# Kernel optimization log

Measured on AMD Instinct MI355X. Metric: run time of the kernel, lower is better.

Reference implementation:

```python
import jax, jax.numpy as jnp
import numpy as np
import math

EPS = 1e-5
GROUPS = 8


def setup_inputs() -> dict:
    key = jax.random.key(0)
    ks = jax.random.split(key, 4)
    b, c, h, w = 4, 256, 64, 64
    x = jax.random.normal(ks[0], (b, c, h, w), dtype=jnp.float32)
    norm_w = jnp.ones((c,), dtype=jnp.float32)
    norm_b = jnp.zeros((c,), dtype=jnp.float32)
    qkv_w = jax.random.normal(ks[1], (3 * c, c), dtype=jnp.float32) * (1.0 / math.sqrt(c))
    qkv_b = jnp.zeros((3 * c,), dtype=jnp.float32)
    proj_w = jax.random.normal(ks[2], (c, c), dtype=jnp.float32) * (1.0 / math.sqrt(c))
    proj_b = jnp.zeros((c,), dtype=jnp.float32)
    return {"x": x, "norm_w": norm_w, "norm_b": norm_b, "qkv_w": qkv_w,
            "qkv_b": qkv_b, "proj_w": proj_w, "proj_b": proj_b}


def group_norm(x, weight, bias):
    b, c, h, w = x.shape
    xg = x.reshape(b, GROUPS, c // GROUPS, h, w)
    mean = xg.mean(axis=(2, 3, 4), keepdims=True)
    var = xg.var(axis=(2, 3, 4), keepdims=True)
    xg = (xg - mean) * jax.lax.rsqrt(var + EPS)
    xn = xg.reshape(b, c, h, w)
    return xn * weight[None, :, None, None] + bias[None, :, None, None]


def reference(x, norm_w, norm_b, qkv_w, qkv_b, proj_w, proj_b):
    b, c, h, w = x.shape
    n = h * w
    xn = group_norm(x, norm_w, norm_b)
    # 1x1 conv == per-pixel linear: tokens [b, n, c]
    tokens = xn.reshape(b, c, n).transpose(0, 2, 1)
    qkv = jnp.einsum('bnc,oc->bno', tokens, qkv_w) + qkv_b  # [b, n, 3c]
    q, k, v = jnp.split(qkv, 3, axis=-1)
    scale = 1.0 / math.sqrt(c)
    attn = jnp.einsum('bqc,bkc->bqk', q, k) * scale  # [b, n, n]
    attn = jax.nn.softmax(attn, axis=-1)
    out = jnp.einsum('bqk,bkc->bqc', attn, v)  # [b, n, c]
    out = jnp.einsum('bnc,oc->bno', out, proj_w) + proj_b
    out = out.transpose(0, 2, 1).reshape(b, c, h, w)
    return x + out
```

## Files before the change

### kernel.cpp

```cpp
#include <hip/hip_runtime.h>
#include <math.h>

typedef unsigned short u16;
typedef __bf16 bf16x8 __attribute__((ext_vector_type(8)));
typedef u16    u16x8  __attribute__((ext_vector_type(8)));
typedef float  f32x4  __attribute__((ext_vector_type(4)));
typedef float  f32x16 __attribute__((ext_vector_type(16)));

__device__ __forceinline__ float b2f(u16 u) {
    union { unsigned u; float f; } x; x.u = ((unsigned)u) << 16; return x.f;
}
__device__ __forceinline__ u16 f2b(float f) {
    union { float f; unsigned u; } x; x.f = f;
    unsigned r = x.u + 0x7FFFu + ((x.u >> 16) & 1u);
    return (u16)(r >> 16);
}
__device__ __forceinline__ f32x4 mfma16(bf16x8 a, bf16x8 b, f32x4 c) {
    return __builtin_amdgcn_mfma_f32_16x16x32_bf16(a, b, c, 0, 0, 0);
}
__device__ __forceinline__ f32x16 mfma32(bf16x8 a, bf16x8 b, f32x16 c) {
    return __builtin_amdgcn_mfma_f32_32x32x16_bf16(a, b, c, 0, 0, 0);
}
__device__ __forceinline__ void dma16(const void* g, void* l) {
    __builtin_amdgcn_global_load_lds((const __attribute__((address_space(1))) void*)g,
                                     (__attribute__((address_space(3))) void*)l, 16, 0, 0);
}
__device__ __forceinline__ int dtype_vote(const unsigned* w) {
    unsigned v = w[threadIdx.x & 63];
    unsigned e = ((v & 0xFFFFu) >> 7) & 0xFFu;
    unsigned long long m = __ballot(e >= 0x60u && e <= 0x8Fu);
    return (__popcll(m) >= 32) ? 0 : 1;
}

#define QSCALE 0.09016844f

__global__ __launch_bounds__(256) void k_cvtx(const void* __restrict__ src, u16* __restrict__ dst,
                                              int* __restrict__ flag, float2* __restrict__ part) {
    const int f = dtype_vote((const unsigned*)src);
    if (blockIdx.x == 0 && threadIdx.x == 0) *flag = f;
    const int i = (blockIdx.x * 256 + threadIdx.x) * 4;
    u16 o[4];
    if (f) {
        float4 v = *(const float4*)((const float*)src + i);
        o[0] = f2b(v.x); o[1] = f2b(v.y); o[2] = f2b(v.z); o[3] = f2b(v.w);
    } else {
        uint2 v = *(const uint2*)((const u16*)src + i);
        o[0] = (u16)(v.x & 0xFFFF); o[1] = (u16)(v.x >> 16);
        o[2] = (u16)(v.y & 0xFFFF); o[3] = (u16)(v.y >> 16);
    }
    unsigned lo = (unsigned)o[0] | ((unsigned)o[1] << 16);
    unsigned hi = (unsigned)o[2] | ((unsigned)o[3] << 16);
    *(uint2*)(dst + i) = make_uint2(lo, hi);
    float s = 0.f, ss = 0.f;
#pragma unroll
    for (int e = 0; e < 4; e++) { float x = b2f(o[e]); s += x; ss += x * x; }
#pragma unroll
    for (int d = 1; d < 64; d <<= 1) { s += __shfl_xor(s, d, 64); ss += __shfl_xor(ss, d, 64); }
    __shared__ float rs[4], rss[4];
    const int wv = threadIdx.x >> 6;
    if ((threadIdx.x & 63) == 0) { rs[wv] = s; rss[wv] = ss; }
    __syncthreads();
    if (threadIdx.x == 0)
        part[blockIdx.x] = make_float2(rs[0] + rs[1] + rs[2] + rs[3],
                                       rss[0] + rss[1] + rss[2] + rss[3]);
}

__global__ __launch_bounds__(64) void k_statsf(const float2* __restrict__ part, float* __restrict__ stats) {
    const int g = blockIdx.x, lane = threadIdx.x;
    float2 a = part[g * 128 + lane], b = part[g * 128 + 64 + lane];
    float s = a.x + b.x, ss = a.y + b.y;
#pragma unroll
    for (int d = 1; d < 64; d <<= 1) { s += __shfl_xor(s, d, 64); ss += __shfl_xor(ss, d, 64); }
    if (lane == 0) {
        float mean = s * (1.f / 131072.f);
        float var = fmaxf(ss * (1.f / 131072.f) - mean * mean, 0.f);
        stats[g] = mean;
        stats[32 + g] = rsqrtf(var + 1e-5f);
    }
}

__global__ __launch_bounds__(256) void k_cvtp(const void* s0, const void* s1, const void* s2,
                                              const void* s3, const void* s4, const void* s5,
                                              u16* d0, u16* d1, u16* d2, u16* d3, u16* d4, u16* d5) {
    const int f = dtype_vote((const unsigned*)s2);
    const int i = blockIdx.x * 256 + threadIdx.x;
    const void* s; u16* d; int j;
    if      (i < 256)    { s = s0; d = d0; j = i; }
    else if (i < 512)    { s = s1; d = d1; j = i - 256; }
    else if (i < 197120) { s = s2; d = d2; j = i - 512; }
    else if (i < 197888) { s = s3; d = d3; j = i - 197120; }
    else if (i < 263424) { s = s4; d = d4; j = i - 197888; }
    else if (i < 263680) { s = s5; d = d5; j = i - 263424; }
    else return;
    if (f) d[j] = f2b(((const float*)s)[j]);
    else   d[j] = ((const u16*)s)[j];
}

__global__ __launch_bounds__(256) void k_tok(const u16* __restrict__ x, const u16* __restrict__ nw,
                                             const u16* __restrict__ nb, const float* __restrict__ stats,
                                             u16* __restrict__ tok) {
    const int b = blockIdx.z, c0 = blockIdx.y * 64, p0 = blockIdx.x * 64;
    __shared__ u16 t[64][72];
    const int cl = threadIdx.x >> 2, seg = threadIdx.x & 3;
    const int c = c0 + cl;
    const int g = c >> 5;
    const float mean = stats[b * 8 + g], rstd = stats[32 + b * 8 + g];
    const float scale = b2f(nw[c]) * rstd;
    const float shift = b2f(nb[c]) - mean * scale;
    const u16* xp = x + ((size_t)(b * 256 + c)) * 4096 + p0 + seg * 16;
#pragma unroll
    for (int h = 0; h < 2; h++) {
        bf16x8 v = *(const bf16x8*)(xp + h * 8);
#pragma unroll
        for (int j = 0; j < 8; j++)
            t[seg * 16 + h * 8 + j][cl] = f2b((float)v[j] * scale + shift);
    }
    __syncthreads();
    u16x8 o0, o1;
#pragma unroll
    for (int j = 0; j < 8; j++) { o0[j] = t[cl][seg * 16 + j]; o1[j] = t[cl][seg * 16 + 8 + j]; }
    u16* op = tok + ((size_t)(b * 4096 + p0 + cl)) * 256 + c0 + seg * 16;
    *(u16x8*)op = o0;
    *((u16x8*)op + 1) = o1;
}

__global__ __launch_bounds__(256) void k_qkv(const u16* __restrict__ A, const u16* __restrict__ W,
                                             const u16* __restrict__ bias,
                                             u16* __restrict__ Qo, u16* __restrict__ Ko, u16* __restrict__ Vt) {
    const int m0 = blockIdx.x * 128, n0 = blockIdx.y * 128;
    const int cls = blockIdx.y >> 1, sub = (blockIdx.y & 1) * 128;
    const int b = m0 >> 12, p0 = m0 & 4095;
    const int tid = threadIdx.x, w = tid >> 6, lane = tid & 63, l15 = lane & 15, l4 = lane >> 4;
    const int wm = w >> 1, wn = w & 1;
    __shared__ __attribute__((aligned(16))) char QL[32768];
    u16* At = (u16*)QL;
    u16* Bt = (u16*)(QL + 16384);
    u16* E  = (u16*)QL;
    f32x4 acc[4][4];
    const f32x4 z = {0.f, 0.f, 0.f, 0.f};
#pragma unroll
    for (int i = 0; i < 4; i++)
#pragma unroll
        for (int j = 0; j < 4; j++) acc[i][j] = z;

    for (int kt = 0; kt < 4; kt++) {
        const int k0 = kt * 64;
#pragma unroll
        for (int i = 0; i < 4; i++) {
            int v = tid + i * 256;
            int row = v >> 3, c8 = v & 7;
            int swz = (c8 ^ (row & 7)) << 3;
            *(u16x8*)(&At[row * 64 + swz]) = *(const u16x8*)(A + (size_t)(m0 + row) * 256 + k0 + c8 * 8);
            *(u16x8*)(&Bt[row * 64 + swz]) = *(const u16x8*)(W + (size_t)(n0 + row) * 256 + k0 + c8 * 8);
        }
        __syncthreads();
#pragma unroll
        for (int ks = 0; ks < 2; ks++) {
            const int sc = ((ks * 4 + l4) ^ (l15 & 7)) << 3;
            bf16x8 af[4], bfr[4];
#pragma unroll
            for (int i = 0; i < 4; i++) {
                af[i]  = *(const bf16x8*)(&At[(wm * 64 + i * 16 + l15) * 64 + sc]);
                bfr[i] = *(const bf16x8*)(&Bt[(wn * 64 + i * 16 + l15) * 64 + sc]);
            }
#pragma unroll
            for (int i = 0; i < 4; i++)
#pragma unroll
                for (int j = 0; j < 4; j++) acc[i][j] = mfma16(af[i], bfr[j], acc[i][j]);
        }
        __syncthreads();
    }

    const float sf = (cls == 0) ? QSCALE : 1.f;
#pragma unroll
    for (int j = 0; j < 4; j++) {
        const int nl = wn * 64 + j * 16 + l15;
        const float bia = b2f(bias[n0 + nl]);
#pragma unroll
        for (int i = 0; i < 4; i++) {
#pragma unroll
            for (int r = 0; r < 4; r++) {
                const int ml = wm * 64 + i * 16 + l4 * 4 + r;
                const u16 val = f2b((acc[i][j][r] + bia) * sf);
                if (cls < 2) {
                    E[ml * 128 + (((nl >> 3) ^ (ml & 7)) << 3) + (nl & 7)] = val;
                } else {
                    int ps = ml ^ ((((ml >> 2) ^ (ml >> 3)) & 1) * 12);
                    E[nl * 128 + (((ps >> 3) ^ (nl & 7)) << 3) + (ps & 7)] = val;
                }
            }
        }
    }
    __syncthreads();
    const int row = tid >> 1, half = tid & 1;
    if (cls < 2) {
        u16* dst = (cls == 0 ? Qo : Ko) + (size_t)(m0 + row) * 256 + sub;
#pragma unroll
        for (int k = 0; k < 8; k++) {
            const int chunk = half * 8 + k;
            u16x8 v = *(const u16x8*)(&E[row * 128 + ((chunk ^ (row & 7)) << 3)]);
            *(u16x8*)(dst + chunk * 8) = v;
        }
    } else {
        u16* dst = Vt + (size_t)(b * 256 + sub + row) * 4096 + p0;
#pragma unroll
        for (int k = 0; k < 8; k++) {
            const int chunk = half * 8 + k;
            u16x8 v = *(const u16x8*)(&E[row * 128 + ((chunk ^ (row & 7)) << 3)]);
            *(u16x8*)(dst + chunk * 8) = v;
        }
    }
}

__global__ __launch_bounds__(256, 2) void k_attn(const u16* __restrict__ Q, const u16* __restrict__ K,
                                                 const u16* __restrict__ Vt,
                                                 u16* __restrict__ Up, float* __restrict__ ml) {
    const int qt = blockIdx.x, b = blockIdx.y, sp = blockIdx.z;
    const int tid = threadIdx.x, w = tid >> 6, lane = tid & 63;
    const int l31 = lane & 31, h = lane >> 5;
    const int qcol = qt * 128 + w * 32 + l31;

    __shared__ __attribute__((aligned(16))) char LB[65536];
    u16* KT = (u16*)LB;
    u16* VT = (u16*)(LB + 16384);

    bf16x8 aq[16];
    {
        const u16* qp = Q + ((size_t)(b * 4096 + qcol)) * 256 + h * 8;
#pragma unroll
        for (int kb = 0; kb < 16; kb++) aq[kb] = *(const bf16x8*)(qp + kb * 16);
    }
    f32x16 acc[8];
#pragma unroll
    for (int ct = 0; ct < 8; ct++)
#pragma unroll
        for (int r = 0; r < 16; r++) acc[ct][r] = 0.f;
    float m_i = -3e38f, l_i = 0.f;

    const u16* Kg0 = K + (size_t)(b * 4096 + sp * 1024) * 256;
    const u16* Vg0 = Vt + (size_t)b * 256 * 4096 + sp * 1024;
    const int wb = (tid & 192) * 8;

    for (int kt = 0; kt < 32; kt++) {
        {
            const u16* Kg = Kg0 + (size_t)kt * 32 * 256;
#pragma unroll
            for (int i = 0; i < 4; i++) {
                int q = i * 256 + tid;
                int row = q >> 5, c = q & 31;
                dma16(Kg + row * 256 + ((c ^ row) << 3), &KT[i * 2048 + wb]);
            }
            const u16* Vg = Vg0 + kt * 32;
#pragma unroll
            for (int i = 0; i < 4; i++) {
                int q = i * 256 + tid;
                int row = q >> 2, c = q & 3;
                dma16(Vg + (size_t)row * 4096 + ((c ^ ((row >> 3) & 3)) << 3), &VT[i * 2048 + wb]);
            }
        }
        __syncthreads();

        f32x16 st;
#pragma unroll
        for (int r = 0; r < 16; r++) st[r] = 0.f;
#pragma unroll
        for (int kb = 0; kb < 16; kb++) {
            bf16x8 bk = *(const bf16x8*)(&KT[l31 * 256 + (((kb * 2 + h) ^ l31) << 3)]);
            st = mfma32(bk, aq[kb], st);
        }

        float mx = st[0];
#pragma unroll
        for (int r = 1; r < 16; r++) mx = fmaxf(mx, st[r]);
        mx = fmaxf(mx, __shfl_xor(mx, 32, 64));
        if (__any(mx > m_i + 4.f)) {
            const float m_new = fmaxf(m_i, mx);
            const float al = __builtin_amdgcn_exp2f(m_i - m_new);
#pragma unroll
            for (int ct = 0; ct < 8; ct++)
#pragma unroll
                for (int r = 0; r < 16; r++) acc[ct][r] *= al;
            l_i *= al;
            m_i = m_new;
        }
        float sum = 0.f;
#pragma unroll
        for (int r = 0; r < 16; r++) {
            st[r] = __builtin_amdgcn_exp2f(st[r] - m_i);
            sum += st[r];
        }
        sum += __shfl_xor(sum, 32, 64);
        l_i += sum;

        union { u16x8 u; bf16x8 bv; } p0, p1;
#pragma unroll
        for (int e = 0; e < 8; e++) { p0.u[e] = f2b(st[e]); p1.u[e] = f2b(st[8 + e]); }

#pragma unroll
        for (int ct = 0; ct < 8; ct++) {
            bf16x8 av0 = *(const bf16x8*)(&VT[(ct * 32 + l31) * 32 + ((h ^ (l31 >> 3)) << 3)]);
            acc[ct] = mfma32(av0, p0.bv, acc[ct]);
            bf16x8 av1 = *(const bf16x8*)(&VT[(ct * 32 + l31) * 32 + (((2 + h) ^ (l31 >> 3)) << 3)]);
            acc[ct] = mfma32(av1, p1.bv, acc[ct]);
        }
        __syncthreads();
    }

    if (h == 0)
        ((float2*)ml)[(size_t)(sp * 4 + b) * 4096 + qcol] = make_float2(m_i, l_i);
    u16* Ot = (u16*)(LB + w * 16384);
#pragma unroll
    for (int ct = 0; ct < 8; ct++) {
#pragma unroll
        for (int r = 0; r < 16; r++) {
            const int c = ct * 32 + (r & 3) + 8 * (r >> 2) + 4 * h;
            Ot[l31 * 256 + (((c >> 3) ^ l31) << 3) + (c & 7)] = f2b(acc[ct][r]);
        }
    }
    u16* up = Up + ((size_t)(sp * 4 + b) * 4096 + qt * 128 + w * 32) * 256;
#pragma unroll
    for (int v = 0; v < 16; v++) {
        int idx = v * 64 + lane;
        int qrow = idx >> 5, c8 = idx & 31;
        u16x8 d = *(const u16x8*)(&Ot[qrow * 256 + ((c8 ^ qrow) << 3)]);
        *(u16x8*)(up + (size_t)qrow * 256 + c8 * 8) = d;
    }
}

__global__ __launch_bounds__(256) void k_proj(const u16* __restrict__ Up, const float* __restrict__ ml,
                                              const u16* __restrict__ W, const u16* __restrict__ bias,
                                              const u16* __restrict__ x, void* __restrict__ out,
                                              const int* __restrict__ flag) {
    const int f32out = *flag;
    const int m0 = blockIdx.x * 64;
    const int b = m0 >> 12, q0 = m0 & 4095;
    const int tid = threadIdx.x, w = tid >> 6, lane = tid & 63, l15 = lane & 15, l4 = lane >> 4;
    const int wm = w >> 1, wn = w & 1;
    __shared__ __attribute__((aligned(16))) char PL[40960];
    u16* At = (u16*)PL;
    u16* Bt = (u16*)(PL + 8192);
    u16* Ot = (u16*)PL;
    __shared__ float4 W4s[64];

    if (tid < 64) {
        const int q = q0 + tid;
        float m_s[4], l_s[4];
#pragma unroll
        for (int s = 0; s < 4; s++) {
            float2 v = ((const float2*)ml)[(size_t)(s * 4 + b) * 4096 + q];
            m_s[s] = v.x; l_s[s] = v.y;
        }
        float M = fmaxf(fmaxf(m_s[0], m_s[1]), fmaxf(m_s[2], m_s[3]));
        float L = 0.f, e[4];
#pragma unroll
        for (int s = 0; s < 4; s++) { e[s] = __builtin_amdgcn_exp2f(m_s[s] - M); L += l_s[s] * e[s]; }
        float inv = 1.f / fmaxf(L, 1e-30f);
        W4s[tid] = make_float4(e[0] * inv, e[1] * inv, e[2] * inv, e[3] * inv);
    }
    __syncthreads();

    const int qa = tid >> 2, ca = (tid & 3) * 16;
    const float4 wq = W4s[qa];
    const float wsv[4] = {wq.x, wq.y, wq.z, wq.w};
    const u16* upb = Up + (size_t)(q0 + qa) * 256 + ca;

    f32x4 acc[2][8];
    const f32x4 z = {0.f, 0.f, 0.f, 0.f};
#pragma unroll
    for (int i = 0; i < 2; i++)
#pragma unroll
        for (int j = 0; j < 8; j++) acc[i][j] = z;

    for (int kt = 0; kt < 4; kt++) {
        const int k0 = kt * 64;
        {
            float vs[16];
#pragma unroll
            for (int e = 0; e < 16; e++) vs[e] = 0.f;
#pragma unroll
            for (int s = 0; s < 4; s++) {
                const u16* p = upb + ((size_t)(s * 4 + b) * 4096) * 256 + k0;
                u16x8 u0 = *(const u16x8*)p;
                u16x8 u1 = *(const u16x8*)(p + 8);
                const float ws = wsv[s];
#pragma unroll
                for (int e = 0; e < 8; e++) { vs[e] += b2f(u0[e]) * ws; vs[8 + e] += b2f(u1[e]) * ws; }
            }
            u16x8 o0, o1;
#pragma unroll
            for (int e = 0; e < 8; e++) { o0[e] = f2b(vs[e]); o1[e] = f2b(vs[8 + e]); }
            const int c8 = ca >> 3;
            *(u16x8*)(&At[qa * 64 + ((c8 ^ (qa & 7)) << 3)]) = o0;
            *(u16x8*)(&At[qa * 64 + (((c8 + 1) ^ (qa & 7)) << 3)]) = o1;
        }
#pragma unroll
        for (int i = 0; i < 8; i++) {
            int v = i * 256 + tid;
            int row = v >> 3, c8 = v & 7;
            *(u16x8*)(&Bt[row * 64 + ((c8 ^ (row & 7)) << 3)]) =
                *(const u16x8*)(W + (size_t)row * 256 + k0 + c8 * 8);
        }
        __syncthreads();
#pragma unroll
        for (int ks = 0; ks < 2; ks++) {
            const int sc = ((ks * 4 + l4) ^ (l15 & 7)) << 3;
            bf16x8 af[2], bfr[8];
#pragma unroll
            for (int i = 0; i < 2; i++)
                af[i] = *(const bf16x8*)(&At[(wm * 32 + i * 16 + l15) * 64 + sc]);
#pragma unroll
            for (int j = 0; j < 8; j++)
                bfr[j] = *(const bf16x8*)(&Bt[(wn * 128 + j * 16 + l15) * 64 + sc]);
#pragma unroll
            for (int i = 0; i < 2; i++)
#pragma unroll
                for (int j = 0; j < 8; j++) acc[i][j] = mfma16(af[i], bfr[j], acc[i][j]);
        }
        __syncthreads();
    }

#pragma unroll
    for (int j = 0; j < 8; j++) {
        const int n = wn * 128 + j * 16 + l15;
        const float bia = b2f(bias[n]);
#pragma unroll
        for (int i = 0; i < 2; i++) {
#pragma unroll
            for (int r = 0; r < 4; r++) {
                const int p = wm * 32 + i * 16 + l4 * 4 + r;
                Ot[n * 64 + ((((p >> 3) ^ (n & 7)) << 3)) + (p & 7)] = f2b(acc[i][j][r] + bia);
            }
        }
    }
    __syncthreads();
    const int ps = (tid & 7) * 8;
#pragma unroll
    for (int v = 0; v < 8; v++) {
        const int n = v * 32 + (tid >> 3);
        u16x8 d = *(const u16x8*)(&Ot[n * 64 + ((((ps >> 3) ^ (n & 7)) << 3))]);
        const size_t base = ((size_t)(b * 256 + n)) * 4096 + q0 + ps;
        u16x8 xv = *(const u16x8*)(x + base);
        if (f32out) {
            float4 o0, o1;
#pragma unroll
            for (int e = 0; e < 4; e++) o0[e] = b2f(d[e]) + b2f(xv[e]);
#pragma unroll
            for (int e = 0; e < 4; e++) o1[e] = b2f(d[4 + e]) + b2f(xv[4 + e]);
            *(float4*)((float*)out + base) = o0;
            *(float4*)((float*)out + base + 4) = o1;
        } else {
            u16x8 o;
#pragma unroll
            for (int e = 0; e < 8; e++) o[e] = f2b(b2f(d[e]) + b2f(xv[e]));
            *(u16x8*)((u16*)out + base) = o;
        }
    }
}

extern "C" void kernel_launch(void* const* d_in, const int* in_sizes, int n_in,
                              void* d_out, int out_size, void* d_ws, size_t ws_size,
                              hipStream_t stream) {
    char* ws = (char*)d_ws;
    float* stats = (float*)ws;
    int*   flag  = (int*)(ws + 2048);
    float2* part = (float2*)(ws + 4096);
    u16* xb  = (u16*)(ws + 65536);
    u16* nwb = xb + (size_t)4194304;
    u16* nbb = nwb + 256;
    u16* qbb = nbb + 256;
    u16* pbb = qbb + 768;
    u16* pad = pbb + 256;
    u16* qwb = pad + 256;
    u16* pwb = qwb + (size_t)196608;
    u16* tok = pwb + (size_t)65536;
    u16* Qb  = tok + (size_t)16384 * 256;
    u16* Kb  = Qb  + (size_t)16384 * 256;
    u16* Vb  = Kb  + (size_t)16384 * 256;
    u16* Upb = Vb  + (size_t)16384 * 256;
    float* mlb = (float*)(Upb + (size_t)16 * 4096 * 256);

    k_cvtx  <<<dim3(4096), dim3(256), 0, stream>>>(d_in[0], xb, flag, part);
    k_statsf<<<dim3(32), dim3(64), 0, stream>>>(part, stats);
    k_cvtp  <<<dim3(1030), dim3(256), 0, stream>>>(d_in[1], d_in[2], d_in[3], d_in[4], d_in[5], d_in[6],
                                                   nwb, nbb, qwb, qbb, pwb, pbb);

    k_tok <<<dim3(64, 4, 4), dim3(256), 0, stream>>>(xb, nwb, nbb, stats, tok);
    k_qkv <<<dim3(128, 6), dim3(256), 0, stream>>>(tok, qwb, qbb, Qb, Kb, Vb);
    k_attn<<<dim3(32, 4, 4), dim3(256), 0, stream>>>(Qb, Kb, Vb, Upb, mlb);
    k_proj<<<dim3(256), dim3(256), 0, stream>>>(Upb, mlb, pwb, pbb, xb, d_out, flag);
}
```

Baseline: 223.4 us.

## Store split-K attention partials channel-major and merge conversion kernels

The attention kernel now writes its split-K partial outputs directly to global memory in a channel-major layout, one bf16 per query column, instead of staging them through a swizzled LDS tile. This cuts its static LDS from 64KB to 32KB. The projection kernel reads the partials with the matching per-channel strided layout. The x and parameter conversion kernels are fused into one launch to save a launch, and the QKV epilogue branch is simplified. The direct stores are 2-byte and strided per lane, coalesced only across lanes, which may raise store transaction cost, though lower LDS use could allow more occupancy.

Measured after the change: 265.9 us. +19.0%, slower.

```diff
diff --git a/kernel.cpp b/kernel.cpp
--- a/kernel.cpp
+++ b/kernel.cpp
@@ -34,23 +34,41 @@
 
 #define QSCALE 0.09016844f
 
-__global__ __launch_bounds__(256) void k_cvtx(const void* __restrict__ src, u16* __restrict__ dst,
-                                              int* __restrict__ flag, float2* __restrict__ part) {
-    const int f = dtype_vote((const unsigned*)src);
+__global__ __launch_bounds__(256) void k_cvt(const void* __restrict__ xsrc, u16* __restrict__ xdst,
+                                             int* __restrict__ flag, float2* __restrict__ part,
+                                             const void* s0, const void* s1, const void* s2,
+                                             const void* s3, const void* s4, const void* s5,
+                                             u16* d0, u16* d1, u16* d2, u16* d3, u16* d4, u16* d5) {
+    if (blockIdx.x >= 4096) {
+        const int f = dtype_vote((const unsigned*)s2);
+        const int i = (blockIdx.x - 4096) * 256 + threadIdx.x;
+        const void* s; u16* d; int j;
+        if      (i < 256)    { s = s0; d = d0; j = i; }
+        else if (i < 512)    { s = s1; d = d1; j = i - 256; }
+        else if (i < 197120) { s = s2; d = d2; j = i - 512; }
+        else if (i < 197888) { s = s3; d = d3; j = i - 197120; }
+        else if (i < 263424) { s = s4; d = d4; j = i - 197888; }
+        else if (i < 263680) { s = s5; d = d5; j = i - 263424; }
+        else return;
+        if (f) d[j] = f2b(((const float*)s)[j]);
+        else   d[j] = ((const u16*)s)[j];
+        return;
+    }
+    const int f = dtype_vote((const unsigned*)xsrc);
     if (blockIdx.x == 0 && threadIdx.x == 0) *flag = f;
     const int i = (blockIdx.x * 256 + threadIdx.x) * 4;
     u16 o[4];
     if (f) {
-        float4 v = *(const float4*)((const float*)src + i);
+        float4 v = *(const float4*)((const float*)xsrc + i);
         o[0] = f2b(v.x); o[1] = f2b(v.y); o[2] = f2b(v.z); o[3] = f2b(v.w);
     } else {
-        uint2 v = *(const uint2*)((const u16*)src + i);
+        uint2 v = *(const uint2*)((const u16*)xsrc + i);
         o[0] = (u16)(v.x & 0xFFFF); o[1] = (u16)(v.x >> 16);
         o[2] = (u16)(v.y & 0xFFFF); o[3] = (u16)(v.y >> 16);
     }
     unsigned lo = (unsigned)o[0] | ((unsigned)o[1] << 16);
     unsigned hi = (unsigned)o[2] | ((unsigned)o[3] << 16);
-    *(uint2*)(dst + i) = make_uint2(lo, hi);
+    *(uint2*)(xdst + i) = make_uint2(lo, hi);
     float s = 0.f, ss = 0.f;
 #pragma unroll
     for (int e = 0; e < 4; e++) { float x = b2f(o[e]); s += x; ss += x * x; }
@@ -77,23 +95,6 @@
         stats[g] = mean;
         stats[32 + g] = rsqrtf(var + 1e-5f);
     }
-}
-
-__global__ __launch_bounds__(256) void k_cvtp(const void* s0, const void* s1, const void* s2,
-                                              const void* s3, const void* s4, const void* s5,
-                                              u16* d0, u16* d1, u16* d2, u16* d3, u16* d4, u16* d5) {
-    const int f = dtype_vote((const unsigned*)s2);
-    const int i = blockIdx.x * 256 + threadIdx.x;
-    const void* s; u16* d; int j;
-    if      (i < 256)    { s = s0; d = d0; j = i; }
-    else if (i < 512)    { s = s1; d = d1; j = i - 256; }
-    else if (i < 197120) { s = s2; d = d2; j = i - 512; }
-    else if (i < 197888) { s = s3; d = d3; j = i - 197120; }
-    else if (i < 263424) { s = s4; d = d4; j = i - 197888; }
-    else if (i < 263680) { s = s5; d = d5; j = i - 263424; }
-    else return;
-    if (f) d[j] = f2b(((const float*)s)[j]);
-    else   d[j] = ((const u16*)s)[j];
 }
 
 __global__ __launch_bounds__(256) void k_tok(const u16* __restrict__ x, const u16* __restrict__ nw,
@@ -193,22 +194,14 @@
     }
     __syncthreads();
     const int row = tid >> 1, half = tid & 1;
-    if (cls < 2) {
-        u16* dst = (cls == 0 ? Qo : Ko) + (size_t)(m0 + row) * 256 + sub;
-#pragma unroll
-        for (int k = 0; k < 8; k++) {
-            const int chunk = half * 8 + k;
-            u16x8 v = *(const u16x8*)(&E[row * 128 + ((chunk ^ (row & 7)) << 3)]);
-            *(u16x8*)(dst + chunk * 8) = v;
-        }
-    } else {
-        u16* dst = Vt + (size_t)(b * 256 + sub + row) * 4096 + p0;
-#pragma unroll
-        for (int k = 0; k < 8; k++) {
-            const int chunk = half * 8 + k;
-            u16x8 v = *(const u16x8*)(&E[row * 128 + ((chunk ^ (row & 7)) << 3)]);
-            *(u16x8*)(dst + chunk * 8) = v;
-        }
+    u16* dst = (cls == 0) ? (Qo + (size_t)(m0 + row) * 256 + sub)
+             : (cls == 1) ? (Ko + (size_t)(m0 + row) * 256 + sub)
+                          : (Vt + (size_t)(b * 256 + sub + row) * 4096 + p0);
+#pragma unroll
+    for (int k = 0; k < 8; k++) {
+        const int chunk = half * 8 + k;
+        u16x8 v = *(const u16x8*)(&E[row * 128 + ((chunk ^ (row & 7)) << 3)]);
+        *(u16x8*)(dst + chunk * 8) = v;
     }
 }
 
@@ -220,9 +213,8 @@
     const int l31 = lane & 31, h = lane >> 5;
     const int qcol = qt * 128 + w * 32 + l31;
 
-    __shared__ __attribute__((aligned(16))) char LB[65536];
-    u16* KT = (u16*)LB;
-    u16* VT = (u16*)(LB + 16384);
+    __shared__ __attribute__((aligned(16))) u16 KT[32 * 256];
+    __shared__ __attribute__((aligned(16))) u16 VT[256 * 32];
 
     bf16x8 aq[16];
     {
@@ -308,22 +300,14 @@
 
     if (h == 0)
         ((float2*)ml)[(size_t)(sp * 4 + b) * 4096 + qcol] = make_float2(m_i, l_i);
-    u16* Ot = (u16*)(LB + w * 16384);
+    u16* up = Up + (size_t)(sp * 4 + b) * 256 * 4096 + qcol;
 #pragma unroll
     for (int ct = 0; ct < 8; ct++) {
 #pragma unroll
         for (int r = 0; r < 16; r++) {
             const int c = ct * 32 + (r & 3) + 8 * (r >> 2) + 4 * h;
-            Ot[l31 * 256 + (((c >> 3) ^ l31) << 3) + (c & 7)] = f2b(acc[ct][r]);
-        }
-    }
-    u16* up = Up + ((size_t)(sp * 4 + b) * 4096 + qt * 128 + w * 32) * 256;
-#pragma unroll
-    for (int v = 0; v < 16; v++) {
-        int idx = v * 64 + lane;
-        int qrow = idx >> 5, c8 = idx & 31;
-        u16x8 d = *(const u16x8*)(&Ot[qrow * 256 + ((c8 ^ qrow) << 3)]);
-        *(u16x8*)(up + (size_t)qrow * 256 + c8 * 8) = d;
+            up[(size_t)c * 4096] = f2b(acc[ct][r]);
+        }
     }
 }
 
@@ -359,10 +343,10 @@
     }
     __syncthreads();
 
-    const int qa = tid >> 2, ca = (tid & 3) * 16;
-    const float4 wq = W4s[qa];
+    const int q_l = tid & 63, cseg = tid >> 6;
+    const float4 wq = W4s[q_l];
     const float wsv[4] = {wq.x, wq.y, wq.z, wq.w};
-    const u16* upb = Up + (size_t)(q0 + qa) * 256 + ca;
+    const u16* upq = Up + q0 + q_l;
 
     f32x4 acc[2][8];
     const f32x4 z = {0.f, 0.f, 0.f, 0.f};
@@ -373,25 +357,14 @@
 
     for (int kt = 0; kt < 4; kt++) {
         const int k0 = kt * 64;
-        {
-            float vs[16];
-#pragma unroll
-            for (int e = 0; e < 16; e++) vs[e] = 0.f;
-#pragma unroll
-            for (int s = 0; s < 4; s++) {
-                const u16* p = upb + ((size_t)(s * 4 + b) * 4096) * 256 + k0;
-                u16x8 u0 = *(const u16x8*)p;
-                u16x8 u1 = *(const u16x8*)(p + 8);
-                const float ws = wsv[s];
-#pragma unroll
-                for (int e = 0; e < 8; e++) { vs[e] += b2f(u0[e]) * ws; vs[8 + e] += b2f(u1[e]) * ws; }
-            }
-            u16x8 o0, o1;
-#pragma unroll
-            for (int e = 0; e < 8; e++) { o0[e] = f2b(vs[e]); o1[e] = f2b(vs[8 + e]); }
-            const int c8 = ca >> 3;
-            *(u16x8*)(&At[qa * 64 + ((c8 ^ (qa & 7)) << 3)]) = o0;
-            *(u16x8*)(&At[qa * 64 + (((c8 + 1) ^ (qa & 7)) << 3)]) = o1;
+#pragma unroll
+        for (int cc = 0; cc < 16; cc++) {
+            const int c = cseg * 16 + cc;
+            float v = 0.f;
+#pragma unroll
+            for (int s = 0; s < 4; s++)
+                v += b2f(upq[(size_t)((s * 4 + b) * 256 + k0 + c) * 4096]) * wsv[s];
+            At[q_l * 64 + (((c >> 3) ^ (q_l & 7)) << 3) + (c & 7)] = f2b(v);
         }
 #pragma unroll
         for (int i = 0; i < 8; i++) {
@@ -477,15 +450,14 @@
     u16* Kb  = Qb  + (size_t)16384 * 256;
     u16* Vb  = Kb  + (size_t)16384 * 256;
     u16* Upb = Vb  + (size_t)16384 * 256;
-    float* mlb = (float*)(Upb + (size_t)16 * 4096 * 256);
-
-    k_cvtx  <<<dim3(4096), dim3(256), 0, stream>>>(d_in[0], xb, flag, part);
+    float* mlb = (float*)(Upb + (size_t)16 * 256 * 4096);
+
+    k_cvt   <<<dim3(5126), dim3(256), 0, stream>>>(d_in[0], xb, flag, part,
+                                                   d_in[1], d_in[2], d_in[3], d_in[4], d_in[5], d_in[6],
+                                                   nwb, nbb, qwb, qbb, pwb, pbb);
     k_statsf<<<dim3(32), dim3(64), 0, stream>>>(part, stats);
-    k_cvtp  <<<dim3(1030), dim3(256), 0, stream>>>(d_in[1], d_in[2], d_in[3], d_in[4], d_in[5], d_in[6],
-                                                   nwb, nbb, qwb, qbb, pwb, pbb);
-
-    k_tok <<<dim3(64, 4, 4), dim3(256), 0, stream>>>(xb, nwb, nbb, stats, tok);
-    k_qkv <<<dim3(128, 6), dim3(256), 0, stream>>>(tok, qwb, qbb, Qb, Kb, Vb);
-    k_attn<<<dim3(32, 4, 4), dim3(256), 0, stream>>>(Qb, Kb, Vb, Upb, mlb);
-    k_proj<<<dim3(256), dim3(256), 0, stream>>>(Upb, mlb, pwb, pbb, xb, d_out, flag);
-}
+    k_tok   <<<dim3(64, 4, 4), dim3(256), 0, stream>>>(xb, nwb, nbb, stats, tok);
+    k_qkv   <<<dim3(128, 6), dim3(256), 0, stream>>>(tok, qwb, qbb, Qb, Kb, Vb);
+    k_attn  <<<dim3(32, 4, 4), dim3(256), 0, stream>>>(Qb, Kb, Vb, Upb, mlb);
+    k_proj  <<<dim3(256), dim3(256), 0, stream>>>(Upb, mlb, pwb, pbb, xb, d_out, flag);
+}
```
